# Kernel tuning notes

Measured on AMD Instinct MI355X. Metric: run time of the kernel, lower is better.

## Reference

```python
import jax, jax.numpy as jnp
import numpy as np

N_NODES = 100000


def _gcn_norm(src, dst, n_nodes, n_edges):
    # PyG gcn_norm with add_self_loops=False: deg over target (col) index
    ones = jnp.ones((n_edges,), dtype=jnp.float32)
    deg = jax.ops.segment_sum(ones, dst, num_segments=n_nodes)
    dinv = jnp.where(deg > 0, jax.lax.rsqrt(deg), 0.0)
    return dinv[src] * dinv[dst]  # [E]


def _arma_conv(x, src, dst, ew, init_w, root_w, bias, n_nodes):
    # x: [N, Fin]; init_w/root_w: [K, Fin, Fout]; bias: [K, 1, Fout]
    h = jnp.einsum('nf,kfo->kno', x, init_w)          # [K, N, Fout]
    msg = h[:, src, :] * ew[None, :, None]             # [K, E, Fout]
    agg = jax.vmap(lambda m: jax.ops.segment_sum(m, dst, num_segments=n_nodes))(msg)
    out = agg + jnp.einsum('nf,kfo->kno', x, root_w) + bias
    return jax.nn.relu(out).mean(axis=0)               # mean over stacks K


def setup_inputs() -> dict:
    key = jax.random.key(0)
    ks = jax.random.split(key, 8)
    n, e = N_NODES, 3200000
    nfeat, hid, nclass, K = 512, 16, 40, 2
    x = jax.random.normal(ks[0], (n, nfeat), dtype=jnp.float32)
    edge_index = jax.random.randint(ks[1], (2, e), 0, n, dtype=jnp.int32)
    s1 = (1.0 / np.sqrt(nfeat)).astype(np.float32) if isinstance(np.sqrt(nfeat), np.ndarray) else np.float32(1.0 / np.sqrt(nfeat))
    s2 = np.float32(1.0 / np.sqrt(hid))
    iw1 = jax.random.normal(ks[2], (K, nfeat, hid), dtype=jnp.float32) * s1
    rw1 = jax.random.normal(ks[3], (K, nfeat, hid), dtype=jnp.float32) * s1
    b1 = jax.random.normal(ks[4], (K, 1, hid), dtype=jnp.float32) * 0.01
    iw2 = jax.random.normal(ks[5], (K, hid, nclass), dtype=jnp.float32) * s2
    rw2 = jax.random.normal(ks[6], (K, hid, nclass), dtype=jnp.float32) * s2
    b2 = jax.random.normal(ks[7], (K, 1, nclass), dtype=jnp.float32) * 0.01
    return {'x': x, 'edge_index': edge_index, 'iw1': iw1, 'rw1': rw1, 'b1': b1,
            'iw2': iw2, 'rw2': rw2, 'b2': b2}


def reference(x, edge_index, iw1, rw1, b1, iw2, rw2, b2):
    src, dst = edge_index[0], edge_index[1]
    n = N_NODES
    ew = _gcn_norm(src, dst, n, src.shape[0])
    h = _arma_conv(x, src, dst, ew, iw1, rw1, b1, n)   # [N, 16]
    out = _arma_conv(h, src, dst, ew, iw2, rw2, b2, n) # [N, nclass]
    return out
```

## Files before the change

### kernel.cpp

```cpp
#include <hip/hip_runtime.h>


#define TB 256
#define CHA 4096

typedef __attribute__((ext_vector_type(8))) short bf8;
typedef __attribute__((ext_vector_type(4))) float f4;

__device__ inline unsigned short f2bf_rne(float f) {
  unsigned int u = __float_as_uint(f);
  unsigned int r = u + 0x7fffu + ((u >> 16) & 1u);
  return (unsigned short)(r >> 16);
}
__device__ inline float bf2f(unsigned short h) {
  return __uint_as_float(((unsigned int)h) << 16);
}
__device__ inline float bflo(unsigned int u) { return __uint_as_float(u << 16); }
__device__ inline float bfhi(unsigned int u) { return __uint_as_float(u & 0xffff0000u); }
__device__ inline unsigned int bfpack(float lo, float hi) {
  return (unsigned int)f2bf_rne(lo) | ((unsigned int)f2bf_rne(hi) << 16);
}

__global__ __launch_bounds__(TB) void k_countA(const int* __restrict__ dst,
                                               int* __restrict__ ccnt, int E) {
  __shared__ int cnt[256];
  int tid = threadIdx.x;
  cnt[tid] = 0;
  __syncthreads();
  int e0 = blockIdx.x * CHA;
  int e1 = min(e0 + CHA, E);
  for (int e = e0 + tid; e < e1; e += TB) atomicAdd(&cnt[dst[e] >> 9], 1);
  __syncthreads();
  if (cnt[tid] > 0) atomicAdd(&ccnt[tid], cnt[tid]);
}

__global__ __launch_bounds__(256) void k_scanC(const int* __restrict__ ccnt,
                                               int* __restrict__ cbase,
                                               int* __restrict__ ccur) {
  __shared__ int sh[256];
  int tid = threadIdx.x;
  int v = ccnt[tid];
  sh[tid] = v;
  __syncthreads();
  for (int d = 1; d < 256; d <<= 1) {
    int t = (tid >= d) ? sh[tid - d] : 0;
    __syncthreads();
    sh[tid] += t;
    __syncthreads();
  }
  int excl = sh[tid] - v;
  cbase[tid] = excl;
  ccur[tid] = excl;
  if (tid == 255) cbase[256] = sh[255];
}

__global__ __launch_bounds__(TB) void k_binA(const int* __restrict__ src,
                                             const int* __restrict__ dst,
                                             int* __restrict__ ccur,
                                             int2* __restrict__ epairs, int E) {
  __shared__ int cnt[256];
  __shared__ int gb[256];
  int tid = threadIdx.x;
  cnt[tid] = 0;
  __syncthreads();
  int e0 = blockIdx.x * CHA;
  int e1 = min(e0 + CHA, E);
  for (int e = e0 + tid; e < e1; e += TB) atomicAdd(&cnt[dst[e] >> 9], 1);
  __syncthreads();
  int c = cnt[tid];
  if (c > 0) gb[tid] = atomicAdd(&ccur[tid], c);
  __syncthreads();
  cnt[tid] = 0;
  __syncthreads();
  for (int e = e0 + tid; e < e1; e += TB) {
    int dv = dst[e];
    int b = dv >> 9;
    int r = atomicAdd(&cnt[b], 1);
    epairs[gb[b] + r] = make_int2(src[e], dv);
  }
}

__global__ __launch_bounds__(TB) void k_binB(const int2* __restrict__ epairs,
                                             const int* __restrict__ cbase,
                                             int* __restrict__ degi,
                                             int* __restrict__ offsets,
                                             int* __restrict__ srcs, int N) {
  __shared__ int cnt[512];
  __shared__ int pre[512];
  int b = blockIdx.x;
  int n0 = b << 9;
  int tid = threadIdx.x;
  int beg = cbase[b], end = cbase[b + 1];
  int i0 = tid, i1 = tid + 256;
  cnt[i0] = 0; cnt[i1] = 0;
  __syncthreads();
  for (int e = beg + tid; e < end; e += TB) atomicAdd(&cnt[epairs[e].y - n0], 1);
  __syncthreads();
  pre[i0] = cnt[i0]; pre[i1] = cnt[i1];
  __syncthreads();
  for (int d = 1; d < 512; d <<= 1) {
    int t0 = (i0 >= d) ? pre[i0 - d] : 0;
    int t1 = (i1 >= d) ? pre[i1 - d] : 0;
    __syncthreads();
    pre[i0] += t0; pre[i1] += t1;
    __syncthreads();
  }
  int e0 = pre[i0] - cnt[i0];
  int e1x = pre[i1] - cnt[i1];
  if (n0 + i0 < N) { degi[n0 + i0] = cnt[i0]; offsets[n0 + i0] = beg + e0; }
  if (n0 + i1 < N) { degi[n0 + i1] = cnt[i1]; offsets[n0 + i1] = beg + e1x; }
  __syncthreads();
  cnt[i0] = e0; cnt[i1] = e1x;
  __syncthreads();
  for (int e = beg + tid; e < end; e += TB) {
    int2 p = epairs[e];
    int pos = atomicAdd(&cnt[p.y - n0], 1);
    srcs[beg + pos] = p.x;
  }
}

__global__ __launch_bounds__(TB) void k_dinv(const int* __restrict__ degi,
                                             float* __restrict__ dinv, int N) {
  int i = blockIdx.x * TB + threadIdx.x;
  if (i < N) {
    int d = degi[i];
    dinv[i] = d > 0 ? rsqrtf((float)d) : 0.0f;
  }
}

__global__ __launch_bounds__(TB) void k_wsplit(const float* __restrict__ iw1,
                                               const float* __restrict__ rw1,
                                               short* __restrict__ Whi,
                                               short* __restrict__ Wlo) {
  int idx = blockIdx.x * TB + threadIdx.x;
  if (idx >= 32768) return;
  int j = idx & 7;
  int l = (idx >> 3) & 63;
  int t = (idx >> 9) & 3;
  int c = idx >> 11;
  int k = c * 32 + (l >> 4) * 8 + j;
  int n = t * 16 + (l & 15);
  float w;
  if (n < 16)
    w = iw1[k * 16 + n];
  else if (n < 32)
    w = iw1[8192 + k * 16 + (n - 16)];
  else if (n < 48)
    w = rw1[k * 16 + (n - 32)];
  else
    w = rw1[8192 + k * 16 + (n - 48)];
  unsigned short h = f2bf_rne(w);
  float res = w - bf2f(h);
  Whi[idx] = (short)h;
  Wlo[idx] = (short)f2bf_rne(res);
}

__global__ __launch_bounds__(TB) void k_gemm1_mfma(const float* __restrict__ x,
                                                   const short* __restrict__ Whi,
                                                   const short* __restrict__ Wlo,
                                                   const float* __restrict__ dinv,
                                                   unsigned short* __restrict__ Hs,
                                                   float* __restrict__ R, int N) {
  int lane = threadIdx.x & 63;
  int wave = threadIdx.x >> 6;
  int row0 = blockIdx.x * 64 + wave * 16;
  int m = lane & 15, quad = lane >> 4;
  int r = row0 + m;
  bool rv = (r < N);
  const float* xr = x + (size_t)r * 512;

  f4 acc[4];
#pragma unroll
  for (int t = 0; t < 4; t++) acc[t] = (f4){0.f, 0.f, 0.f, 0.f};

  for (int c = 0; c < 16; ++c) {
    float xv[8];
    if (rv) {
      f4 a0 = *(const f4*)(xr + c * 32 + quad * 8);
      f4 a1 = *(const f4*)(xr + c * 32 + quad * 8 + 4);
      xv[0] = a0.x; xv[1] = a0.y; xv[2] = a0.z; xv[3] = a0.w;
      xv[4] = a1.x; xv[5] = a1.y; xv[6] = a1.z; xv[7] = a1.w;
    } else {
#pragma unroll
      for (int j = 0; j < 8; ++j) xv[j] = 0.f;
    }
    bf8 ahi, alo;
#pragma unroll
    for (int j = 0; j < 8; ++j) {
      unsigned short h = f2bf_rne(xv[j]);
      float res = xv[j] - bf2f(h);
      ahi[j] = (short)h;
      alo[j] = (short)f2bf_rne(res);
    }
    const short* wb = Whi + ((size_t)(c * 4) * 64 + lane) * 8;
    const short* wl = Wlo + ((size_t)(c * 4) * 64 + lane) * 8;
#pragma unroll
    for (int t = 0; t < 4; ++t) {
      bf8 bh = *(const bf8*)(wb + t * 512);
      bf8 bl = *(const bf8*)(wl + t * 512);
      acc[t] = __builtin_amdgcn_mfma_f32_16x16x32_bf16(ahi, bh, acc[t], 0, 0, 0);
      acc[t] = __builtin_amdgcn_mfma_f32_16x16x32_bf16(alo, bh, acc[t], 0, 0, 0);
      acc[t] = __builtin_amdgcn_mfma_f32_16x16x32_bf16(ahi, bl, acc[t], 0, 0, 0);
    }
  }
  float dv[4];
#pragma unroll
  for (int g = 0; g < 4; ++g) {
    int ro = row0 + quad * 4 + g;
    dv[g] = (ro < N) ? dinv[ro] : 0.f;
  }
#pragma unroll
  for (int t = 0; t < 4; ++t) {
#pragma unroll
    for (int g = 0; g < 4; ++g) {
      int ro = row0 + quad * 4 + g;
      if (ro < N) {
        if (t < 2)
          Hs[(size_t)ro * 32 + t * 16 + m] = f2bf_rne(acc[t][g] * dv[g]);
        else
          R[(size_t)ro * 32 + (t - 2) * 16 + m] = acc[t][g];
      }
    }
  }
}

__global__ __launch_bounds__(TB) void k_prop1(const int* __restrict__ offsets,
                                              const int* __restrict__ degi,
                                              const int* __restrict__ srcs,
                                              const unsigned short* __restrict__ Hs,
                                              const float* __restrict__ R,
                                              const float* __restrict__ dinv,
                                              const float* __restrict__ b1,
                                              float* __restrict__ h,
                                              unsigned short* __restrict__ hs, int N) {
  int tid = blockIdx.x * TB + threadIdx.x;
  int q = tid & 3;
  int n = tid >> 2;
  if (n >= N) return;
  int beg = offsets[n], cnt = degi[n];
  float a[8];
#pragma unroll
  for (int j = 0; j < 8; j++) a[j] = 0.f;
  for (int i = 0; i < cnt; i++) {
    int s = srcs[beg + i];
    uint4 v = *(const uint4*)(Hs + (size_t)s * 32 + q * 8);
    a[0] += bflo(v.x); a[1] += bfhi(v.x);
    a[2] += bflo(v.y); a[3] += bfhi(v.y);
    a[4] += bflo(v.z); a[5] += bfhi(v.z);
    a[6] += bflo(v.w); a[7] += bfhi(v.w);
  }
  float dvn = dinv[n];
  f4 r0 = *(const f4*)(R + (size_t)n * 32 + q * 8);
  f4 r1 = *(const f4*)(R + (size_t)n * 32 + q * 8 + 4);
  float rr[8] = {r0.x, r0.y, r0.z, r0.w, r1.x, r1.y, r1.z, r1.w};
  float vv[8];
#pragma unroll
  for (int j = 0; j < 8; j++) {
    int f = q * 8 + j;
    vv[j] = fmaxf(a[j] * dvn + rr[j] + b1[(f >> 4) * 16 + (f & 15)], 0.f);
  }
  float pv[8];
#pragma unroll
  for (int j = 0; j < 8; j++) pv[j] = __shfl_xor(vv[j], 2);
  if (q < 2) {
    float hv[8];
#pragma unroll
    for (int j = 0; j < 8; j++) hv[j] = 0.5f * (vv[j] + pv[j]);
    f4 o0 = {hv[0], hv[1], hv[2], hv[3]};
    f4 o1 = {hv[4], hv[5], hv[6], hv[7]};
    *(f4*)(h + (size_t)n * 16 + q * 8) = o0;
    *(f4*)(h + (size_t)n * 16 + q * 8 + 4) = o1;
    uint4 ob;
    ob.x = bfpack(hv[0] * dvn, hv[1] * dvn);
    ob.y = bfpack(hv[2] * dvn, hv[3] * dvn);
    ob.z = bfpack(hv[4] * dvn, hv[5] * dvn);
    ob.w = bfpack(hv[6] * dvn, hv[7] * dvn);
    *(uint4*)(hs + (size_t)n * 16 + q * 8) = ob;
  }
}

__global__ __launch_bounds__(TB) void k_prop2(const int* __restrict__ offsets,
                                              const int* __restrict__ degi,
                                              const int* __restrict__ srcs,
                                              const unsigned short* __restrict__ hs,
                                              const float* __restrict__ dinv,
                                              float* __restrict__ Ah, int N) {
  int tid = blockIdx.x * TB + threadIdx.x;
  int q = tid & 3;
  int n = tid >> 2;
  if (n >= N) return;
  int beg = offsets[n], cnt = degi[n];
  float a[4] = {0.f, 0.f, 0.f, 0.f};
  for (int i = 0; i < cnt; i++) {
    int s = srcs[beg + i];
    uint2 v = *(const uint2*)(hs + (size_t)s * 16 + q * 4);
    a[0] += bflo(v.x); a[1] += bfhi(v.x);
    a[2] += bflo(v.y); a[3] += bfhi(v.y);
  }
  float dvn = dinv[n];
  f4 o = {a[0] * dvn, a[1] * dvn, a[2] * dvn, a[3] * dvn};
  *(f4*)(Ah + (size_t)n * 16 + q * 4) = o;
}

__global__ __launch_bounds__(TB) void k_final(const float* __restrict__ Ah,
                                              const float* __restrict__ h,
                                              const float* __restrict__ iw2,
                                              const float* __restrict__ rw2,
                                              const float* __restrict__ b2,
                                              float* __restrict__ out, int N) {
  __shared__ float w_iw[2 * 16 * 40];
  __shared__ float w_rw[2 * 16 * 40];
  __shared__ float w_b[2 * 40];
  for (int i = threadIdx.x; i < 1280; i += TB) {
    w_iw[i] = iw2[i];
    w_rw[i] = rw2[i];
  }
  for (int i = threadIdx.x; i < 80; i += TB) w_b[i] = b2[i];
  __syncthreads();

  int idx = blockIdx.x * TB + threadIdx.x;
  if (idx >= N * 40) return;
  int n = idx / 40;
  int o = idx - n * 40;
  float a[16], hr[16];
#pragma unroll
  for (int f = 0; f < 16; f++) {
    a[f] = Ah[(size_t)n * 16 + f];
    hr[f] = h[(size_t)n * 16 + f];
  }
  float res = 0.f;
#pragma unroll
  for (int k = 0; k < 2; k++) {
    float s = w_b[k * 40 + o];
#pragma unroll
    for (int f = 0; f < 16; f++) {
      s += a[f] * w_iw[(k * 16 + f) * 40 + o];
      s += hr[f] * w_rw[(k * 16 + f) * 40 + o];
    }
    res += fmaxf(s, 0.f);
  }
  out[idx] = 0.5f * res;
}

extern "C" void kernel_launch(void* const* d_in, const int* in_sizes, int n_in,
                              void* d_out, int out_size, void* d_ws, size_t ws_size,
                              hipStream_t stream) {
  const float* x = (const float*)d_in[0];
  const int* ei = (const int*)d_in[1];
  const float* iw1 = (const float*)d_in[2];
  const float* rw1 = (const float*)d_in[3];
  const float* b1 = (const float*)d_in[4];
  const float* iw2 = (const float*)d_in[5];
  const float* rw2 = (const float*)d_in[6];
  const float* b2 = (const float*)d_in[7];
  float* out = (float*)d_out;

  const int N = in_sizes[0] / 512;
  const int E = in_sizes[1] / 2;
  const int* src = ei;
  const int* dst = ei + E;
  const int NC = (N + 511) >> 9;

  char* base = (char*)d_ws;
  size_t off = 0;
  auto alloc = [&](size_t bytes) -> void* {
    off = (off + 255) & ~(size_t)255;
    void* p = base + off;
    off += bytes;
    return p;
  };
  int* degi = (int*)alloc((size_t)N * 4);
  float* dinv = (float*)alloc((size_t)N * 4);
  int* offsets = (int*)alloc((size_t)N * 4);
  int* ccnt = (int*)alloc(260 * 4);
  int* cbase = (int*)alloc(260 * 4);
  int* ccur = (int*)alloc(260 * 4);
  int2* epairs = (int2*)alloc((size_t)E * 8);
  int* srcs = (int*)alloc((size_t)E * 4);
  unsigned short* Hs = (unsigned short*)alloc((size_t)N * 32 * 2);
  float* hbuf = (float*)alloc((size_t)N * 16 * 4);
  unsigned short* hs = (unsigned short*)alloc((size_t)N * 16 * 2);
  float* Ah = (float*)alloc((size_t)N * 16 * 4);
  short* Whi = (short*)alloc(32768 * 2);
  short* Wlo = (short*)alloc(32768 * 2);
  float* R = (float*)epairs;
  (void)ws_size;

  hipMemsetAsync(ccnt, 0, 260 * 4, stream);

  int NBLK = (E + CHA - 1) / CHA;
  k_countA<<<NBLK, TB, 0, stream>>>(dst, ccnt, E);
  k_scanC<<<1, 256, 0, stream>>>(ccnt, cbase, ccur);
  k_binA<<<NBLK, TB, 0, stream>>>(src, dst, ccur, epairs, E);
  k_binB<<<NC, TB, 0, stream>>>(epairs, cbase, degi, offsets, srcs, N);
  k_dinv<<<(N + TB - 1) / TB, TB, 0, stream>>>(degi, dinv, N);
  k_wsplit<<<128, TB, 0, stream>>>(iw1, rw1, Whi, Wlo);
  k_gemm1_mfma<<<(N + 63) / 64, TB, 0, stream>>>(x, Whi, Wlo, dinv, Hs, R, N);
  k_prop1<<<((size_t)N * 4 + TB - 1) / TB, TB, 0, stream>>>(offsets, degi, srcs, Hs, R,
                                                            dinv, b1, hbuf, hs, N);
  k_prop2<<<((size_t)N * 4 + TB - 1) / TB, TB, 0, stream>>>(offsets, degi, srcs, hs,
                                                            dinv, Ah, N);
  k_final<<<((size_t)N * 40 + TB - 1) / TB, TB, 0, stream>>>(Ah, hbuf, iw2, rw2, b2, out, N);
}
```

Before: 603.4 us.

## Pack edge pairs into 32-bit words, fuse dinv into binB, unroll gathers

Edge pairs written during binning are packed into a single 32-bit word holding the source index shifted left by 9 bits plus the low 9 bits of the destination. This halves the intermediate edge buffer traffic in binA and binB. The degree-inverse computation is folded into binB, which removes one kernel launch. Both propagation kernels now prefetch source indices four at a time and issue four gathers per iteration to raise memory-level parallelism, at the cost of more registers and a packing that assumes src fits in 23 bits.

```diff
diff --git a/kernel.cpp b/kernel.cpp
--- a/kernel.cpp
+++ b/kernel.cpp
@@ -20,6 +20,20 @@
 __device__ inline unsigned int bfpack(float lo, float hi) {
   return (unsigned int)f2bf_rne(lo) | ((unsigned int)f2bf_rne(hi) << 16);
 }
+
+#define ACC8(v)                                   \
+  do {                                            \
+    a[0] += bflo((v).x); a[1] += bfhi((v).x);     \
+    a[2] += bflo((v).y); a[3] += bfhi((v).y);     \
+    a[4] += bflo((v).z); a[5] += bfhi((v).z);     \
+    a[6] += bflo((v).w); a[7] += bfhi((v).w);     \
+  } while (0)
+
+#define ACC4(v)                                   \
+  do {                                            \
+    a[0] += bflo((v).x); a[1] += bfhi((v).x);     \
+    a[2] += bflo((v).y); a[3] += bfhi((v).y);     \
+  } while (0)
 
 __global__ __launch_bounds__(TB) void k_countA(const int* __restrict__ dst,
                                                int* __restrict__ ccnt, int E) {
@@ -57,7 +71,8 @@
 __global__ __launch_bounds__(TB) void k_binA(const int* __restrict__ src,
                                              const int* __restrict__ dst,
                                              int* __restrict__ ccur,
-                                             int2* __restrict__ epairs, int E) {
+                                             unsigned int* __restrict__ epairs,
+                                             int E) {
   __shared__ int cnt[256];
   __shared__ int gb[256];
   int tid = threadIdx.x;
@@ -76,15 +91,16 @@
     int dv = dst[e];
     int b = dv >> 9;
     int r = atomicAdd(&cnt[b], 1);
-    epairs[gb[b] + r] = make_int2(src[e], dv);
-  }
-}
-
-__global__ __launch_bounds__(TB) void k_binB(const int2* __restrict__ epairs,
+    epairs[gb[b] + r] = ((unsigned int)src[e] << 9) | (unsigned int)(dv & 511);
+  }
+}
+
+__global__ __launch_bounds__(TB) void k_binB(const unsigned int* __restrict__ epairs,
                                              const int* __restrict__ cbase,
                                              int* __restrict__ degi,
                                              int* __restrict__ offsets,
-                                             int* __restrict__ srcs, int N) {
+                                             int* __restrict__ srcs,
+                                             float* __restrict__ dinv, int N) {
   __shared__ int cnt[512];
   __shared__ int pre[512];
   int b = blockIdx.x;
@@ -94,7 +110,8 @@
   int i0 = tid, i1 = tid + 256;
   cnt[i0] = 0; cnt[i1] = 0;
   __syncthreads();
-  for (int e = beg + tid; e < end; e += TB) atomicAdd(&cnt[epairs[e].y - n0], 1);
+  for (int e = beg + tid; e < end; e += TB)
+    atomicAdd(&cnt[epairs[e] & 511u], 1);
   __syncthreads();
   pre[i0] = cnt[i0]; pre[i1] = cnt[i1];
   __syncthreads();
@@ -107,24 +124,25 @@
   }
   int e0 = pre[i0] - cnt[i0];
   int e1x = pre[i1] - cnt[i1];
-  if (n0 + i0 < N) { degi[n0 + i0] = cnt[i0]; offsets[n0 + i0] = beg + e0; }
-  if (n0 + i1 < N) { degi[n0 + i1] = cnt[i1]; offsets[n0 + i1] = beg + e1x; }
+  if (n0 + i0 < N) {
+    int c0 = cnt[i0];
+    degi[n0 + i0] = c0;
+    offsets[n0 + i0] = beg + e0;
+    dinv[n0 + i0] = c0 > 0 ? rsqrtf((float)c0) : 0.0f;
+  }
+  if (n0 + i1 < N) {
+    int c1 = cnt[i1];
+    degi[n0 + i1] = c1;
+    offsets[n0 + i1] = beg + e1x;
+    dinv[n0 + i1] = c1 > 0 ? rsqrtf((float)c1) : 0.0f;
+  }
   __syncthreads();
   cnt[i0] = e0; cnt[i1] = e1x;
   __syncthreads();
   for (int e = beg + tid; e < end; e += TB) {
-    int2 p = epairs[e];
-    int pos = atomicAdd(&cnt[p.y - n0], 1);
-    srcs[beg + pos] = p.x;
-  }
-}
-
-__global__ __launch_bounds__(TB) void k_dinv(const int* __restrict__ degi,
-                                             float* __restrict__ dinv, int N) {
-  int i = blockIdx.x * TB + threadIdx.x;
-  if (i < N) {
-    int d = degi[i];
-    dinv[i] = d > 0 ? rsqrtf((float)d) : 0.0f;
+    unsigned int p = epairs[e];
+    int pos = atomicAdd(&cnt[p & 511u], 1);
+    srcs[beg + pos] = (int)(p >> 9);
   }
 }
 
@@ -238,17 +256,38 @@
   int n = tid >> 2;
   if (n >= N) return;
   int beg = offsets[n], cnt = degi[n];
+  const unsigned short* Hq = Hs + q * 8;
   float a[8];
 #pragma unroll
   for (int j = 0; j < 8; j++) a[j] = 0.f;
-  for (int i = 0; i < cnt; i++) {
+
+  int i = 0;
+  if (cnt >= 4) {
+    int s0 = srcs[beg], s1 = srcs[beg + 1], s2 = srcs[beg + 2], s3 = srcs[beg + 3];
+    for (; i + 8 <= cnt; i += 4) {
+      uint4 v0 = *(const uint4*)(Hq + (size_t)s0 * 32);
+      uint4 v1 = *(const uint4*)(Hq + (size_t)s1 * 32);
+      uint4 v2 = *(const uint4*)(Hq + (size_t)s2 * 32);
+      uint4 v3 = *(const uint4*)(Hq + (size_t)s3 * 32);
+      s0 = srcs[beg + i + 4]; s1 = srcs[beg + i + 5];
+      s2 = srcs[beg + i + 6]; s3 = srcs[beg + i + 7];
+      ACC8(v0); ACC8(v1); ACC8(v2); ACC8(v3);
+    }
+    {
+      uint4 v0 = *(const uint4*)(Hq + (size_t)s0 * 32);
+      uint4 v1 = *(const uint4*)(Hq + (size_t)s1 * 32);
+      uint4 v2 = *(const uint4*)(Hq + (size_t)s2 * 32);
+      uint4 v3 = *(const uint4*)(Hq + (size_t)s3 * 32);
+      ACC8(v0); ACC8(v1); ACC8(v2); ACC8(v3);
+      i += 4;
+    }
+  }
+  for (; i < cnt; ++i) {
     int s = srcs[beg + i];
-    uint4 v = *(const uint4*)(Hs + (size_t)s * 32 + q * 8);
-    a[0] += bflo(v.x); a[1] += bfhi(v.x);
-    a[2] += bflo(v.y); a[3] += bfhi(v.y);
-    a[4] += bflo(v.z); a[5] += bfhi(v.z);
-    a[6] += bflo(v.w); a[7] += bfhi(v.w);
-  }
+    uint4 v = *(const uint4*)(Hq + (size_t)s * 32);
+    ACC8(v);
+  }
+
   float dvn = dinv[n];
   f4 r0 = *(const f4*)(R + (size_t)n * 32 + q * 8);
   f4 r1 = *(const f4*)(R + (size_t)n * 32 + q * 8 + 4);
@@ -290,13 +329,36 @@
   int n = tid >> 2;
   if (n >= N) return;
   int beg = offsets[n], cnt = degi[n];
+  const unsigned short* Hq = hs + q * 4;
   float a[4] = {0.f, 0.f, 0.f, 0.f};
-  for (int i = 0; i < cnt; i++) {
+
+  int i = 0;
+  if (cnt >= 4) {
+    int s0 = srcs[beg], s1 = srcs[beg + 1], s2 = srcs[beg + 2], s3 = srcs[beg + 3];
+    for (; i + 8 <= cnt; i += 4) {
+      uint2 v0 = *(const uint2*)(Hq + (size_t)s0 * 16);
+      uint2 v1 = *(const uint2*)(Hq + (size_t)s1 * 16);
+      uint2 v2 = *(const uint2*)(Hq + (size_t)s2 * 16);
+      uint2 v3 = *(const uint2*)(Hq + (size_t)s3 * 16);
+      s0 = srcs[beg + i + 4]; s1 = srcs[beg + i + 5];
+      s2 = srcs[beg + i + 6]; s3 = srcs[beg + i + 7];
+      ACC4(v0); ACC4(v1); ACC4(v2); ACC4(v3);
+    }
+    {
+      uint2 v0 = *(const uint2*)(Hq + (size_t)s0 * 16);
+      uint2 v1 = *(const uint2*)(Hq + (size_t)s1 * 16);
+      uint2 v2 = *(const uint2*)(Hq + (size_t)s2 * 16);
+      uint2 v3 = *(const uint2*)(Hq + (size_t)s3 * 16);
+      ACC4(v0); ACC4(v1); ACC4(v2); ACC4(v3);
+      i += 4;
+    }
+  }
+  for (; i < cnt; ++i) {
     int s = srcs[beg + i];
-    uint2 v = *(const uint2*)(hs + (size_t)s * 16 + q * 4);
-    a[0] += bflo(v.x); a[1] += bfhi(v.x);
-    a[2] += bflo(v.y); a[3] += bfhi(v.y);
-  }
+    uint2 v = *(const uint2*)(Hq + (size_t)s * 16);
+    ACC4(v);
+  }
+
   float dvn = dinv[n];
   f4 o = {a[0] * dvn, a[1] * dvn, a[2] * dvn, a[3] * dvn};
   *(f4*)(Ah + (size_t)n * 16 + q * 4) = o;
@@ -375,7 +437,10 @@
   int* ccnt = (int*)alloc(260 * 4);
   int* cbase = (int*)alloc(260 * 4);
   int* ccur = (int*)alloc(260 * 4);
-  int2* epairs = (int2*)alloc((size_t)E * 8);
+  size_t epair_bytes = (size_t)E * 4;
+  size_t r_bytes = (size_t)N * 32 * 4;
+  unsigned int* epairs =
+      (unsigned int*)alloc(epair_bytes > r_bytes ? epair_bytes : r_bytes);
   int* srcs = (int*)alloc((size_t)E * 4);
   unsigned short* Hs = (unsigned short*)alloc((size_t)N * 32 * 2);
   float* hbuf = (float*)alloc((size_t)N * 16 * 4);
@@ -392,8 +457,7 @@
   k_countA<<<NBLK, TB, 0, stream>>>(dst, ccnt, E);
   k_scanC<<<1, 256, 0, stream>>>(ccnt, cbase, ccur);
   k_binA<<<NBLK, TB, 0, stream>>>(src, dst, ccur, epairs, E);
-  k_binB<<<NC, TB, 0, stream>>>(epairs, cbase, degi, offsets, srcs, N);
-  k_dinv<<<(N + TB - 1) / TB, TB, 0, stream>>>(degi, dinv, N);
+  k_binB<<<NC, TB, 0, stream>>>(epairs, cbase, degi, offsets, srcs, dinv, N);
   k_wsplit<<<128, TB, 0, stream>>>(iw1, rw1, Whi, Wlo);
   k_gemm1_mfma<<<(N + 63) / 64, TB, 0, stream>>>(x, Whi, Wlo, dinv, Hs, R, N);
   k_prop1<<<((size_t)N * 4 + TB - 1) / TB, TB, 0, stream>>>(offsets, degi, srcs, Hs, R,
```

New measurement: 565.9 us. 1.07x faster.
